# Performance work log

Hardware: AMD Instinct MI355X
Metric: run time of the kernel (lower is better)

## Reference

```python
import jax, jax.numpy as jnp
import numpy as np

B, N, C, H = 2, 2048, 1024, 16
D = C // H  # head_dim = 64


def setup_inputs() -> dict:
    key = jax.random.key(0)
    k1, k2, k3, k4 = jax.random.split(key, 4)
    x = jax.random.normal(k1, (B, N, C), dtype=jnp.float32)
    # params (torch Linear: y = x @ W.T + b). Store as [in, out] for einsum.
    w_qkv = jax.random.normal(k2, (C, 3 * C), dtype=jnp.float32) * (1.0 / np.sqrt(C))
    w_out = jax.random.normal(k3, (C, C), dtype=jnp.float32) * (1.0 / np.sqrt(C))
    b_out = jax.random.normal(k4, (C,), dtype=jnp.float32) * 0.01
    # causal mask: 1 above the diagonal -> masked_fill(-inf)
    attn_mask = jnp.triu(jnp.ones((N, N), dtype=jnp.int32), k=1)
    return {"x": x, "w_qkv": w_qkv, "w_out": w_out, "b_out": b_out, "attn_mask": attn_mask}


def reference(x, w_qkv, w_out, b_out, attn_mask):
    b, n, c = x.shape
    scale = 1.0 / jnp.sqrt(jnp.asarray(D, dtype=x.dtype))
    qkv = jnp.einsum('bnc,cd->bnd', x, w_qkv)                # [B, N, 3C]
    qkv = qkv.reshape(b, n, 3, H, D)
    q = qkv[:, :, 0].transpose(0, 2, 1, 3)                   # [B, H, N, D]
    k = qkv[:, :, 1].transpose(0, 2, 1, 3)
    v = qkv[:, :, 2].transpose(0, 2, 1, 3)
    scores = jnp.einsum('bhqd,bhkd->bhqk', q, k) * scale     # [B, H, N, N]
    scores = jnp.where(attn_mask == 1, jnp.asarray(-jnp.inf, dtype=scores.dtype), scores)
    attn = jax.nn.softmax(scores, axis=-1)
    # dropout is identity in eval mode (deterministic reference)
    out = jnp.einsum('bhqk,bhkd->bhqd', attn, v)             # [B, H, N, D]
    out = out.transpose(0, 2, 1, 3).reshape(b, n, c)         # [B, N, C]
    return jnp.einsum('bnc,cd->bnd', out, w_out) + b_out
```

## Files before the change

kernel.cpp:

```cpp
#include <hip/hip_runtime.h>

typedef _Float16 f16;
typedef _Float16 f16x8 __attribute__((ext_vector_type(8)));
typedef _Float16 f16x4 __attribute__((ext_vector_type(4)));
typedef float    f32x4 __attribute__((ext_vector_type(4)));

#define MFMA16(a, b, c) __builtin_amdgcn_mfma_f32_16x16x32_f16((a), (b), (c), 0, 0, 0)

__device__ __forceinline__ void gload16(const void* g, void* l) {
  __builtin_amdgcn_global_load_lds(
      (const __attribute__((address_space(1))) unsigned int*)g,
      (__attribute__((address_space(3))) unsigned int*)l, 16, 0, 0);
}

__device__ __forceinline__ float ex2(float x) {
  float r;
  asm("v_exp_f32 %0, %1" : "=v"(r) : "v"(x));
  return r;
}

#define WAITV(N) asm volatile("s_waitcnt vmcnt(" #N ")" ::: "memory")
#define BARRIER() __builtin_amdgcn_s_barrier()
#define CFENCE() asm volatile("" ::: "memory")


__global__ void cast_f32_f16(const float* __restrict__ in, f16* __restrict__ out, int n4) {
  int i = blockIdx.x * blockDim.x + threadIdx.x;
  if (i < n4) {
    float4 v = ((const float4*)in)[i];
    f16x4 o;
    o.x = (f16)v.x; o.y = (f16)v.y; o.z = (f16)v.z; o.w = (f16)v.w;
    ((f16x4*)out)[i] = o;
  }
}

__global__ void transpose_cast(const float* __restrict__ in, f16* __restrict__ out, int R, int Cc) {
  __shared__ float tile[32][33];
  int c0 = blockIdx.x * 32, r0 = blockIdx.y * 32;
  int tx = threadIdx.x, ty = threadIdx.y;
#pragma unroll
  for (int i = ty; i < 32; i += 8)
    tile[i][tx] = in[(size_t)(r0 + i) * Cc + c0 + tx];
  __syncthreads();
#pragma unroll
  for (int i = ty; i < 32; i += 8)
    out[(size_t)(c0 + i) * R + r0 + tx] = (f16)tile[tx][i];
}

template <int KDIM>
__device__ __forceinline__ void gemm_core(const f16* __restrict__ A, const f16* __restrict__ Bt,
                                          int bm, int bn, f16* lA, f16* lB, f32x4 acc[4][4]) {
  const int t = threadIdx.x, lane = t & 63, wave = t >> 6;
  const int wm = wave >> 1, wn = wave & 1;
  const int srow = lane >> 3;
  const int skb = (lane & 7) * 16;
  const int nkt = KDIM / 64;

  auto STAGE = [&](int buf, int kt) {
#pragma unroll
    for (int c = 0; c < 4; ++c) {
      int cc = c * 4 + wave;
      int row = cc * 8 + srow;
      int kbs = skb ^ ((row & 7) << 4);
      gload16((const char*)A + (size_t)(bm * 128 + row) * (KDIM * 2) + kt * 128 + kbs,
              lA + buf * 8192 + cc * 512);
      gload16((const char*)Bt + (size_t)(bn * 128 + row) * (KDIM * 2) + kt * 128 + kbs,
              lB + buf * 8192 + cc * 512);
    }
  };

  STAGE(0, 0);
  if (nkt > 1) STAGE(1, 1);
  for (int kt = 0; kt < nkt; ++kt) {
    int cur = kt & 1;
    if (kt + 1 < nkt) WAITV(8); else WAITV(0);
    BARRIER();
    const f16* A0 = lA + cur * 8192;
    const f16* B0 = lB + cur * 8192;
    __builtin_amdgcn_s_setprio(1);
#pragma unroll
    for (int ks = 0; ks < 2; ++ks) {
      f16x8 af[4], bf[4];
#pragma unroll
      for (int mi = 0; mi < 4; ++mi) {
        int r = wm * 64 + mi * 16 + (lane & 15);
        int ke = (ks * 32 + ((lane >> 4) << 3)) ^ ((r & 7) << 3);
        af[mi] = *(const f16x8*)&A0[r * 64 + ke];
      }
#pragma unroll
      for (int ni = 0; ni < 4; ++ni) {
        int r = wn * 64 + ni * 16 + (lane & 15);
        int ke = (ks * 32 + ((lane >> 4) << 3)) ^ ((r & 7) << 3);
        bf[ni] = *(const f16x8*)&B0[r * 64 + ke];
      }
#pragma unroll
      for (int mi = 0; mi < 4; ++mi)
#pragma unroll
        for (int ni = 0; ni < 4; ++ni)
          acc[mi][ni] = MFMA16(af[mi], bf[ni], acc[mi][ni]);
    }
    __builtin_amdgcn_s_setprio(0);
    BARRIER();
    CFENCE();
    if (kt + 2 < nkt) STAGE(cur, kt + 2);
  }
}

__global__ __launch_bounds__(256, 2) void gemm_qkv(const f16* __restrict__ A,
                                                   const f16* __restrict__ Bt,
                                                   f16* __restrict__ Qo, f16* __restrict__ Ko,
                                                   f16* __restrict__ Vt) {
  __shared__ __align__(16) f16 lA[2 * 8192];
  __shared__ __align__(16) f16 lB[2 * 8192];
  f32x4 acc[4][4] = {};
  int w = blockIdx.x;
  int xcd = w & 7, i = w >> 3;
  int xr = xcd >> 1, xc = xcd & 1;
  int bm = xr * 8 + (i & 7);
  int bn = xc * 12 + (i >> 3);
  gemm_core<1024>(A, Bt, bm, bn, lA, lB, acc);
  int lane = threadIdx.x & 63, wave = threadIdx.x >> 6;
  int wm = wave >> 1, wn = wave & 1;
  int sec = (bn * 128) >> 10;
  float scl = (sec == 0) ? 0.18033688f : 1.0f;
#pragma unroll
  for (int mi = 0; mi < 4; ++mi)
#pragma unroll
    for (int ni = 0; ni < 4; ++ni)
#pragma unroll
      for (int reg = 0; reg < 4; ++reg) {
        int gr = bm * 128 + wm * 64 + mi * 16 + ((lane >> 4) << 2) + reg;
        int gc = bn * 128 + wn * 64 + ni * 16 + (lane & 15);
        int b = gr >> 11, n = gr & 2047;
        int jj = gc & 1023;
        int h = jj >> 6, d = jj & 63;
        f16 v = (f16)(acc[mi][ni][reg] * scl);
        size_t bh = (size_t)(b * 16 + h);
        if (sec == 0)      Qo[(bh * 2048 + n) * 64 + d] = v;
        else if (sec == 1) Ko[(bh * 2048 + n) * 64 + d] = v;
        else {
          int np = (n & ~31) | (((n >> 2) & 3) << 3) | (((n >> 4) & 1) << 2) | (n & 3);
          Vt[(bh * 64 + d) * 2048 + np] = v;
        }
      }
}

__device__ __forceinline__ void attn_one(const f16* __restrict__ Qb, const f16* __restrict__ Kb,
                                         const f16* __restrict__ Vb, f16* __restrict__ Ob,
                                         int qt, int lane, int wave, f16* lK, f16* lV) {
  const int N = 2048;
  const int wq0 = qt * 64 + wave * 16;
  const int g = lane >> 4, q15 = lane & 15;
  f16x8 qf[2];
#pragma unroll
  for (int ks = 0; ks < 2; ++ks)
    qf[ks] = *(const f16x8*)&Qb[(size_t)(wq0 + q15) * 64 + ks * 32 + (g << 3)];
  f32x4 oacc[4] = {};
  float mrun = -1e30f, lrun = 0.f;
  const int srow = lane >> 3, skb = (lane & 7) * 16;
  const int ntiles = (qt >> 1) + 1;

  auto STAGE = [&](int buf, int kv) {
    int kv0 = kv << 7;
#pragma unroll
    for (int c = 0; c < 4; ++c) {
      int cc = c * 4 + wave;
      {
        int row = cc * 8 + srow;
        int kbs = skb ^ ((row & 7) << 4);
        gload16((const char*)Kb + (size_t)(kv0 + row) * 128 + kbs, lK + buf * 8192 + cc * 512);
      }
      {
        int sv = cc >> 3, c8 = cc & 7;
        int row = c8 * 8 + srow;
        int kbs = skb ^ ((row & 7) << 4);
        gload16((const char*)Vb + (size_t)row * (N * 2) + (size_t)(kv0 + sv * 64) * 2 + kbs,
                lV + buf * 8192 + sv * 4096 + c8 * 512);
      }
    }
  };

  STAGE(0, 0);
  if (ntiles > 1) STAGE(1, 1);
  for (int kv = 0; kv < ntiles; ++kv) {
    int cur = kv & 1;
    if (kv + 1 < ntiles) WAITV(8); else WAITV(0);
    BARRIER();
    const f16* K0 = lK + cur * 8192;
    const f16* V0 = lV + cur * 8192;
    int kv0 = kv << 7;
    f32x4 s[8] = {};
    __builtin_amdgcn_s_setprio(1);
#pragma unroll
    for (int ks = 0; ks < 2; ++ks) {
      f16x8 kf[8];
#pragma unroll
      for (int ni = 0; ni < 8; ++ni) {
        int r = ni * 16 + q15;
        int ke = (ks * 32 + (g << 3)) ^ ((r & 7) << 3);
        kf[ni] = *(const f16x8*)&K0[r * 64 + ke];
      }
#pragma unroll
      for (int ni = 0; ni < 8; ++ni) s[ni] = MFMA16(kf[ni], qf[ks], s[ni]);
    }
    __builtin_amdgcn_s_setprio(0);
    if (kv == ntiles - 1) {
      int gq = wq0 + q15;
#pragma unroll
      for (int ni = 0; ni < 8; ++ni)
#pragma unroll
        for (int reg = 0; reg < 4; ++reg) {
          int gk = kv0 + ni * 16 + g * 4 + reg;
          if (gk > gq) s[ni][reg] = -1e30f;
        }
    }
    f32x4 m4 = s[0];
#pragma unroll
    for (int ni = 1; ni < 8; ++ni)
#pragma unroll
      for (int reg = 0; reg < 4; ++reg) m4[reg] = fmaxf(m4[reg], s[ni][reg]);
    float mx = fmaxf(fmaxf(m4[0], m4[1]), fmaxf(m4[2], m4[3]));
    mx = fmaxf(mx, __shfl_xor(mx, 16));
    mx = fmaxf(mx, __shfl_xor(mx, 32));
    if (__any(mx > mrun)) {
      float mnew = fmaxf(mrun, mx);
      float corr = ex2(mrun - mnew);
      mrun = mnew;
      lrun *= corr;
#pragma unroll
      for (int ni = 0; ni < 4; ++ni)
#pragma unroll
        for (int reg = 0; reg < 4; ++reg) oacc[ni][reg] *= corr;
    }
    float rsum = 0.f;
#pragma unroll
    for (int ni = 0; ni < 8; ++ni)
#pragma unroll
      for (int reg = 0; reg < 4; ++reg) {
        float p = ex2(s[ni][reg] - mrun);
        s[ni][reg] = p;
        rsum += p;
      }
    rsum += __shfl_xor(rsum, 16);
    rsum += __shfl_xor(rsum, 32);
    lrun += rsum;
    f16x8 pf[4];
#pragma unroll
    for (int ks = 0; ks < 4; ++ks)
#pragma unroll
      for (int e = 0; e < 8; ++e) pf[ks][e] = (f16)s[2 * ks + (e >> 2)][e & 3];
    __builtin_amdgcn_s_setprio(1);
#pragma unroll
    for (int ks = 0; ks < 4; ++ks) {
      const f16* Vs = V0 + (ks >> 1) * 4096;
      f16x8 vf[4];
#pragma unroll
      for (int mi = 0; mi < 4; ++mi) {
        int r = mi * 16 + q15;
        int ke = ((ks & 1) * 32 + (g << 3)) ^ ((r & 7) << 3);
        vf[mi] = *(const f16x8*)&Vs[r * 64 + ke];
      }
#pragma unroll
      for (int mi = 0; mi < 4; ++mi) oacc[mi] = MFMA16(vf[mi], pf[ks], oacc[mi]);
    }
    __builtin_amdgcn_s_setprio(0);
    BARRIER();
    CFENCE();
    if (kv + 2 < ntiles) STAGE(cur, kv + 2);
  }
  float inv = 1.0f / lrun;
  int gq = wq0 + q15;
#pragma unroll
  for (int mi = 0; mi < 4; ++mi) {
    f16x4 o4;
#pragma unroll
    for (int reg = 0; reg < 4; ++reg) o4[reg] = (f16)(oacc[mi][reg] * inv);
    *(f16x4*)&Ob[(size_t)gq * 1024 + mi * 16 + g * 4] = o4;
  }
}

__global__ __launch_bounds__(256, 2) void attn(const f16* __restrict__ Q,
                                               const f16* __restrict__ K,
                                               const f16* __restrict__ Vt,
                                               f16* __restrict__ O) {
  __shared__ __align__(16) f16 lK[2 * 8192];
  __shared__ __align__(16) f16 lV[2 * 8192];
  int w = blockIdx.x;
  int c = w & 7, j = w >> 3;
  int bh = c * 4 + (j >> 4);
  int x = j & 15;
  int b = bh >> 4, h = bh & 15;
  int lane = threadIdx.x & 63, wave = threadIdx.x >> 6;
  const f16* Qb = Q + (size_t)bh * 2048 * 64;
  const f16* Kb = K + (size_t)bh * 2048 * 64;
  const f16* Vb = Vt + (size_t)bh * 2048 * 64;
  f16* Ob = O + (size_t)b * 2048 * 1024 + h * 64;
  attn_one(Qb, Kb, Vb, Ob, 31 - x, lane, wave, lK, lV);
  attn_one(Qb, Kb, Vb, Ob, x, lane, wave, lK, lV);
}

__global__ __launch_bounds__(256, 2) void gemm_out(const f16* __restrict__ A,
                                                   const f16* __restrict__ Bt,
                                                   const float* __restrict__ bias,
                                                   float* __restrict__ out) {
  __shared__ __align__(16) f16 lA[2 * 8192];
  __shared__ __align__(16) f16 lB[2 * 8192];
  f32x4 acc[4][4] = {};
  int w = blockIdx.x;
  int xcd = w & 7, i = w >> 3;
  int bm = xcd * 4 + (i & 3);
  int bn = i >> 2;
  gemm_core<1024>(A, Bt, bm, bn, lA, lB, acc);
  int lane = threadIdx.x & 63, wave = threadIdx.x >> 6;
  int wm = wave >> 1, wn = wave & 1;
#pragma unroll
  for (int mi = 0; mi < 4; ++mi)
#pragma unroll
    for (int ni = 0; ni < 4; ++ni)
#pragma unroll
      for (int reg = 0; reg < 4; ++reg) {
        int gr = bm * 128 + wm * 64 + mi * 16 + ((lane >> 4) << 2) + reg;
        int gc = bn * 128 + wn * 64 + ni * 16 + (lane & 15);
        out[(size_t)gr * 1024 + gc] = acc[mi][ni][reg] + bias[gc];
      }
}

extern "C" void kernel_launch(void* const* d_in, const int* in_sizes, int n_in,
                              void* d_out, int out_size, void* d_ws, size_t ws_size,
                              hipStream_t stream) {
  const float* x     = (const float*)d_in[0];
  const float* w_qkv = (const float*)d_in[1];
  const float* w_out = (const float*)d_in[2];
  const float* b_out = (const float*)d_in[3];
  float* out = (float*)d_out;
  char* ws = (char*)d_ws;

  f16* xh    = (f16*)(ws);
  f16* wqkvT = (f16*)(ws + (8u << 20));
  f16* woutT = (f16*)(ws + (14u << 20));
  f16* Qs    = (f16*)(ws + (16u << 20));
  f16* Ks    = (f16*)(ws + (24u << 20));
  f16* Vts   = (f16*)(ws + (32u << 20));
  f16* Oa    = (f16*)(ws + (40u << 20));

  cast_f32_f16<<<4096, 256, 0, stream>>>(x, xh, 1048576);
  transpose_cast<<<dim3(96, 32), dim3(32, 8), 0, stream>>>(w_qkv, wqkvT, 1024, 3072);
  transpose_cast<<<dim3(32, 32), dim3(32, 8), 0, stream>>>(w_out, woutT, 1024, 1024);
  gemm_qkv<<<768, 256, 0, stream>>>(xh, wqkvT, Qs, Ks, Vts);
  attn<<<512, 256, 0, stream>>>(Qs, Ks, Vts, Oa);
  gemm_out<<<256, 256, 0, stream>>>(Oa, woutT, b_out, out);
}
```

Baseline: 118.6 us.

## Single-buffer GEMM staging and transpose V via LDS for coalesced stores

Replaces the double-buffered async LDS pipeline in the shared GEMM core with a single-buffered load, sync, compute loop, and drops the priority hints. This halves LDS use, which may allow more blocks per CU, but global loads are no longer overlapped with MFMA work. The QKV epilogue for the V section now stages the tile in padded LDS with the permuted row order, then writes transposed V rows with 16-byte vector stores instead of scattered 2-byte stores. Q and K stores stay element-wise as before.

Measured after the change: 103.8 us. 1.14x faster.

```diff
diff --git a/kernel.cpp b/kernel.cpp
--- a/kernel.cpp
+++ b/kernel.cpp
@@ -55,29 +55,19 @@
   const int srow = lane >> 3;
   const int skb = (lane & 7) * 16;
   const int nkt = KDIM / 64;
-
-  auto STAGE = [&](int buf, int kt) {
+  for (int kt = 0; kt < nkt; ++kt) {
+    __syncthreads();
 #pragma unroll
     for (int c = 0; c < 4; ++c) {
       int cc = c * 4 + wave;
       int row = cc * 8 + srow;
       int kbs = skb ^ ((row & 7) << 4);
       gload16((const char*)A + (size_t)(bm * 128 + row) * (KDIM * 2) + kt * 128 + kbs,
-              lA + buf * 8192 + cc * 512);
+              lA + cc * 512);
       gload16((const char*)Bt + (size_t)(bn * 128 + row) * (KDIM * 2) + kt * 128 + kbs,
-              lB + buf * 8192 + cc * 512);
-    }
-  };
-
-  STAGE(0, 0);
-  if (nkt > 1) STAGE(1, 1);
-  for (int kt = 0; kt < nkt; ++kt) {
-    int cur = kt & 1;
-    if (kt + 1 < nkt) WAITV(8); else WAITV(0);
-    BARRIER();
-    const f16* A0 = lA + cur * 8192;
-    const f16* B0 = lB + cur * 8192;
-    __builtin_amdgcn_s_setprio(1);
+              lB + cc * 512);
+    }
+    __syncthreads();
 #pragma unroll
     for (int ks = 0; ks < 2; ++ks) {
       f16x8 af[4], bf[4];
@@ -85,13 +75,13 @@
       for (int mi = 0; mi < 4; ++mi) {
         int r = wm * 64 + mi * 16 + (lane & 15);
         int ke = (ks * 32 + ((lane >> 4) << 3)) ^ ((r & 7) << 3);
-        af[mi] = *(const f16x8*)&A0[r * 64 + ke];
+        af[mi] = *(const f16x8*)&lA[r * 64 + ke];
       }
 #pragma unroll
       for (int ni = 0; ni < 4; ++ni) {
         int r = wn * 64 + ni * 16 + (lane & 15);
         int ke = (ks * 32 + ((lane >> 4) << 3)) ^ ((r & 7) << 3);
-        bf[ni] = *(const f16x8*)&B0[r * 64 + ke];
+        bf[ni] = *(const f16x8*)&lB[r * 64 + ke];
       }
 #pragma unroll
       for (int mi = 0; mi < 4; ++mi)
@@ -99,10 +89,6 @@
         for (int ni = 0; ni < 4; ++ni)
           acc[mi][ni] = MFMA16(af[mi], bf[ni], acc[mi][ni]);
     }
-    __builtin_amdgcn_s_setprio(0);
-    BARRIER();
-    CFENCE();
-    if (kt + 2 < nkt) STAGE(cur, kt + 2);
   }
 }
 
@@ -110,8 +96,9 @@
                                                    const f16* __restrict__ Bt,
                                                    f16* __restrict__ Qo, f16* __restrict__ Ko,
                                                    f16* __restrict__ Vt) {
-  __shared__ __align__(16) f16 lA[2 * 8192];
-  __shared__ __align__(16) f16 lB[2 * 8192];
+  __shared__ __align__(16) f16 smem[128 * 136];
+  f16* lA = smem;
+  f16* lB = smem + 8192;
   f32x4 acc[4][4] = {};
   int w = blockIdx.x;
   int xcd = w & 7, i = w >> 3;
@@ -121,28 +108,53 @@
   gemm_core<1024>(A, Bt, bm, bn, lA, lB, acc);
   int lane = threadIdx.x & 63, wave = threadIdx.x >> 6;
   int wm = wave >> 1, wn = wave & 1;
+  int g = lane >> 4, q15 = lane & 15;
   int sec = (bn * 128) >> 10;
-  float scl = (sec == 0) ? 0.18033688f : 1.0f;
-#pragma unroll
-  for (int mi = 0; mi < 4; ++mi)
-#pragma unroll
-    for (int ni = 0; ni < 4; ++ni)
-#pragma unroll
-      for (int reg = 0; reg < 4; ++reg) {
-        int gr = bm * 128 + wm * 64 + mi * 16 + ((lane >> 4) << 2) + reg;
-        int gc = bn * 128 + wn * 64 + ni * 16 + (lane & 15);
-        int b = gr >> 11, n = gr & 2047;
-        int jj = gc & 1023;
-        int h = jj >> 6, d = jj & 63;
-        f16 v = (f16)(acc[mi][ni][reg] * scl);
-        size_t bh = (size_t)(b * 16 + h);
-        if (sec == 0)      Qo[(bh * 2048 + n) * 64 + d] = v;
-        else if (sec == 1) Ko[(bh * 2048 + n) * 64 + d] = v;
-        else {
-          int np = (n & ~31) | (((n >> 2) & 3) << 3) | (((n >> 4) & 1) << 2) | (n & 3);
-          Vt[(bh * 64 + d) * 2048 + np] = v;
+  if (sec < 2) {
+    float scl = (sec == 0) ? 0.18033688f : 1.0f;
+#pragma unroll
+    for (int mi = 0; mi < 4; ++mi)
+#pragma unroll
+      for (int ni = 0; ni < 4; ++ni)
+#pragma unroll
+        for (int reg = 0; reg < 4; ++reg) {
+          int gr = bm * 128 + wm * 64 + mi * 16 + (g << 2) + reg;
+          int gc = bn * 128 + wn * 64 + ni * 16 + q15;
+          int b = gr >> 11, n = gr & 2047;
+          int jj = gc & 1023;
+          int h = jj >> 6, d = jj & 63;
+          f16 v = (f16)(acc[mi][ni][reg] * scl);
+          size_t bh = (size_t)(b * 16 + h);
+          if (sec == 0) Qo[(bh * 2048 + n) * 64 + d] = v;
+          else          Ko[(bh * 2048 + n) * 64 + d] = v;
         }
-      }
+  } else {
+    __syncthreads();
+#pragma unroll
+    for (int mi = 0; mi < 4; ++mi)
+#pragma unroll
+      for (int ni = 0; ni < 4; ++ni)
+#pragma unroll
+        for (int reg = 0; reg < 4; ++reg) {
+          int rl = wm * 64 + mi * 16 + (g << 2) + reg;
+          int cl = wn * 64 + ni * 16 + q15;
+          int r5 = rl & 31;
+          int rlp = (rl & ~31) | (((r5 >> 2) & 3) << 3) | (((r5 >> 4) & 1) << 2) | (r5 & 3);
+          smem[cl * 136 + rlp] = (f16)acc[mi][ni][reg];
+        }
+    __syncthreads();
+    int tid = threadIdx.x;
+    int cl = tid >> 1, half = tid & 1;
+    int jj = (bn * 128 + cl) & 1023;
+    int h = jj >> 6, d = jj & 63;
+    int b = (bm * 128) >> 11;
+    size_t bh = (size_t)(b * 16 + h);
+    f16* dst = Vt + (bh * 64 + d) * 2048 + (bm * 128 & 2047) + half * 64;
+    const f16* src = smem + cl * 136 + half * 64;
+#pragma unroll
+    for (int j8 = 0; j8 < 8; ++j8)
+      *(f16x8*)&dst[j8 * 8] = *(const f16x8*)&src[j8 * 8];
+  }
 }
 
 __device__ __forceinline__ void attn_one(const f16* __restrict__ Qb, const f16* __restrict__ Kb,
@@ -303,8 +315,8 @@
                                                    const f16* __restrict__ Bt,
                                                    const float* __restrict__ bias,
                                                    float* __restrict__ out) {
-  __shared__ __align__(16) f16 lA[2 * 8192];
-  __shared__ __align__(16) f16 lB[2 * 8192];
+  __shared__ __align__(16) f16 lA[128 * 64];
+  __shared__ __align__(16) f16 lB[128 * 64];
   f32x4 acc[4][4] = {};
   int w = blockIdx.x;
   int xcd = w & 7, i = w >> 3;
```
